# Kernel tuning notes

Measured on AMD Instinct MI355X. Metric: run time of the kernel, lower is better.

## Reference

```python
import jax, jax.numpy as jnp
import numpy as np

KS = 63      # Gaussian kernel size (module default)
SIGMA = 32.0 # Gaussian sigma (module default)


def _gaussian_kernel2d(k, sigma):
    # kornia get_gaussian_kernel2d: outer product of normalized 1D gaussians
    x = jnp.arange(k, dtype=jnp.float32) - k // 2
    g = jnp.exp(-(x * x) / (2.0 * sigma * sigma))
    g = g / g.sum()
    return jnp.outer(g, g)  # [k,k]


def _filter2d_constant(x, k2d):
    # kornia filter2d, border_type='constant' (zero pad), depthwise per channel
    C = x.shape[1]
    kern = jnp.broadcast_to(k2d, (C, 1) + k2d.shape)  # [C,1,k,k]
    return jax.lax.conv_general_dilated(
        x, kern, window_strides=(1, 1), padding='SAME',
        dimension_numbers=('NCHW', 'OIHW', 'NCHW'), feature_group_count=C)


def _grid_sample_bilinear(img, grid, align_corners=False):
    # torch.nn.functional.grid_sample, mode='bilinear', padding_mode='zeros'
    B, C, H, W = img.shape
    gx, gy = grid[..., 0], grid[..., 1]
    if align_corners:
        x = (gx + 1.0) * (W - 1) * 0.5
        y = (gy + 1.0) * (H - 1) * 0.5
    else:
        x = ((gx + 1.0) * W - 1.0) * 0.5
        y = ((gy + 1.0) * H - 1.0) * 0.5
    x0 = jnp.floor(x); y0 = jnp.floor(y)
    x0i = x0.astype(jnp.int32); y0i = y0.astype(jnp.int32)
    x1i = x0i + 1; y1i = y0i + 1
    wx1 = x - x0; wx0 = 1.0 - wx1
    wy1 = y - y0; wy0 = 1.0 - wy1

    def gather(iy, ix):
        valid = ((ix >= 0) & (ix < W) & (iy >= 0) & (iy < H))
        iyc = jnp.clip(iy, 0, H - 1)
        ixc = jnp.clip(ix, 0, W - 1)
        # per-batch fancy gather: [B,C,H,W]
        v = jax.vmap(lambda im, yy, xx: im[:, yy, xx])(img, iyc, ixc)
        return v * valid[:, None].astype(img.dtype)

    out = (gather(y0i, x0i) * (wy0 * wx0)[:, None]
           + gather(y0i, x1i) * (wy0 * wx1)[:, None]
           + gather(y1i, x0i) * (wy1 * wx0)[:, None]
           + gather(y1i, x1i) * (wy1 * wx1)[:, None])
    return out


def setup_inputs() -> dict:
    key = jax.random.key(0)
    k1, k2 = jax.random.split(key)
    image = jax.random.normal(k1, (8, 3, 512, 512), dtype=jnp.float32)
    noise = jax.random.uniform(k2, (8, 2, 512, 512), dtype=jnp.float32)
    return {"image": image, "noise": noise}


def reference(image, noise):
    B, C, H, W = image.shape
    noise = noise * 2.0 - 1.0                      # rand*2-1 as in forward()
    k2d = _gaussian_kernel2d(KS, SIGMA)
    disp_xy = _filter2d_constant(noise, k2d)       # [B,2,H,W]
    disp = jnp.transpose(disp_xy, (0, 2, 3, 1))    # [B,H,W,2] (x,y)
    # kornia create_meshgrid(normalized_coordinates=True): linspace(-1,1)
    xs = jnp.linspace(-1.0, 1.0, W, dtype=image.dtype)
    ys = jnp.linspace(-1.0, 1.0, H, dtype=image.dtype)
    base = jnp.stack(jnp.meshgrid(xs, ys, indexing='xy'), axis=-1)  # [H,W,2]
    grid = jnp.clip(base[None] + disp, -1.0, 1.0)
    warped = _grid_sample_bilinear(image, grid, align_corners=False)
    return warped, disp
```

## Files before the change

kernel.cpp:

```cpp
#include <hip/hip_runtime.h>
#include <math.h>

#define KS 63
#define RAD 31
#define NB 8
#define NC 3
#define NH 512
#define NW 512
#define PADH 576

struct GaussW { float w[KS]; };

__global__ __launch_bounds__(256) void hblur_kernel(const float* __restrict__ noise,
                                                    float* __restrict__ tmp, GaussW gw) {
    const int bid = blockIdx.x;
    const int t = threadIdx.x;
    if (bid >= NB * NH) {
        const int pid = bid - NB * NH;
        const int img = pid >> 5;
        const int pr  = pid & 31;
        const int row = (pr < 16) ? (pr * 2) : (544 + (pr - 16) * 2);
        float4* dst = (float4*)(tmp + ((size_t)img * PADH + row) * NW);
        dst[t] = make_float4(0.f, 0.f, 0.f, 0.f);
        return;
    }
    const int b = bid >> 9;
    const int h = bid & (NH - 1);
    const int ch = t >> 7;
    const int tt = t & 127;

    __shared__ float rows[2][PADH];
    const float* src = noise + ((size_t)(b * 2 + ch) * NH + h) * NW;
    {
        const float4 nv = *(const float4*)(src + 4 * tt);
        float4 sv;
        sv.x = fmaf(nv.x, 2.f, -1.f); sv.y = fmaf(nv.y, 2.f, -1.f);
        sv.z = fmaf(nv.z, 2.f, -1.f); sv.w = fmaf(nv.w, 2.f, -1.f);
        *(float4*)&rows[ch][32 + 4 * tt] = sv;
        if (tt < 8) {
            *(float4*)&rows[ch][4 * tt]       = make_float4(0.f, 0.f, 0.f, 0.f);
            *(float4*)&rows[ch][544 + 4 * tt] = make_float4(0.f, 0.f, 0.f, 0.f);
        }
    }
    __syncthreads();

    float acc[4] = {0.f, 0.f, 0.f, 0.f};
#pragma unroll
    for (int c = 0; c < 17; ++c) {
        const float4 v = *(const float4*)&rows[ch][4 * tt + 4 * c];
        const float vv[4] = {v.x, v.y, v.z, v.w};
#pragma unroll
        for (int e = 0; e < 4; ++e) {
#pragma unroll
            for (int oo = 0; oo < 4; ++oo) {
                const int j = 4 * c + e - oo - 1;
                if (j >= 0 && j < KS) acc[oo] = fmaf(vv[e], gw.w[j], acc[oo]);
            }
        }
    }
    float4* dst = (float4*)(tmp + (((size_t)(b * 2 + ch) * PADH) + 32 + h) * NW + 4 * tt);
    *dst = make_float4(acc[0], acc[1], acc[2], acc[3]);
}

__global__ __launch_bounds__(256) void vwarp_kernel(const float* __restrict__ tmp,
                                                    const float* __restrict__ img,
                                                    float2* __restrict__ disp,
                                                    float* __restrict__ warped,
                                                    GaussW gw) {
    const int t = threadIdx.x;
    int bid = blockIdx.x;
    bid = (bid & 7) * 256 + (bid >> 3);
    const int wt = bid & 1;
    const int ht = (bid >> 1) & 127;
    const int b  = bid >> 8;
    const int w  = wt * 256 + t;
    const int h0 = ht * 4;

    const float* c0 = tmp + (((size_t)(b * 2 + 0) * PADH) + h0 + 1) * NW + w;
    const float* c1 = tmp + (((size_t)(b * 2 + 1) * PADH) + h0 + 1) * NW + w;

    float ax[4] = {0.f, 0.f, 0.f, 0.f};
    float ay[4] = {0.f, 0.f, 0.f, 0.f};
#pragma unroll
    for (int rr = 0; rr < 66; ++rr) {
        const float vx = c0[(size_t)rr * NW];
        const float vy = c1[(size_t)rr * NW];
#pragma unroll
        for (int o = 0; o < 4; ++o) {
            const int j = rr - o;
            if (j >= 0 && j < KS) {
                ax[o] = fmaf(vx, gw.w[j], ax[o]);
                ay[o] = fmaf(vy, gw.w[j], ay[o]);
            }
        }
    }

    const float gxb = fmaf((float)w, 2.0f / 511.0f, -1.0f);
    const float* i0 = img + (size_t)b * NC * NH * NW;
    const float* i1 = i0 + NH * NW;
    const float* i2 = i1 + NH * NW;
    float* wp = warped + (size_t)b * NC * NH * NW;

#pragma unroll
    for (int o = 0; o < 4; ++o) {
        const int h = h0 + o;
        disp[((size_t)b * NH + h) * NW + w] = make_float2(ax[o], ay[o]);

        float gx = gxb + ax[o];
        float gy = fmaf((float)h, 2.0f / 511.0f, -1.0f) + ay[o];
        gx = fminf(1.f, fmaxf(-1.f, gx));
        gy = fminf(1.f, fmaxf(-1.f, gy));

        const float x = ((gx + 1.0f) * (float)NW - 1.0f) * 0.5f;
        const float y = ((gy + 1.0f) * (float)NH - 1.0f) * 0.5f;
        const float xf = floorf(x), yf = floorf(y);
        const int x0 = (int)xf, y0 = (int)yf;
        const int x1 = x0 + 1,  y1 = y0 + 1;
        const float wx1 = x - xf, wx0 = 1.0f - wx1;
        const float wy1 = y - yf, wy0 = 1.0f - wy1;
        const float fx0 = ((unsigned)x0 < NW) ? 1.f : 0.f;
        const float fx1 = ((unsigned)x1 < NW) ? 1.f : 0.f;
        const float fy0 = ((unsigned)y0 < NH) ? 1.f : 0.f;
        const float fy1 = ((unsigned)y1 < NH) ? 1.f : 0.f;
        const int x0c = min(max(x0, 0), NW - 1), x1c = min(max(x1, 0), NW - 1);
        const int y0c = min(max(y0, 0), NH - 1), y1c = min(max(y1, 0), NH - 1);
        const float w00 = wy0 * wx0 * (fy0 * fx0), w01 = wy0 * wx1 * (fy0 * fx1);
        const float w10 = wy1 * wx0 * (fy1 * fx0), w11 = wy1 * wx1 * (fy1 * fx1);
        const int o00 = y0c * NW + x0c, o01 = y0c * NW + x1c;
        const int o10 = y1c * NW + x0c, o11 = y1c * NW + x1c;
        const size_t po = (size_t)h * NW + w;
        wp[po]               = ((i0[o00] * w00 + i0[o01] * w01) + i0[o10] * w10) + i0[o11] * w11;
        wp[NH * NW + po]     = ((i1[o00] * w00 + i1[o01] * w01) + i1[o10] * w10) + i1[o11] * w11;
        wp[2 * NH * NW + po] = ((i2[o00] * w00 + i2[o01] * w01) + i2[o10] * w10) + i2[o11] * w11;
    }
}

extern "C" void kernel_launch(void* const* d_in, const int* in_sizes, int n_in,
                              void* d_out, int out_size, void* d_ws, size_t ws_size,
                              hipStream_t stream) {
    const float* image = (const float*)d_in[0];
    const float* noise = (const float*)d_in[1];
    float* warped = (float*)d_out;
    float* dispo  = (float*)d_out + (size_t)NB * NC * NH * NW;
    float* scratch = (float*)d_ws;

    GaussW gw;
    float s = 0.f;
    for (int i = 0; i < KS; ++i) {
        const float xv = (float)(i - RAD);
        gw.w[i] = expf(-(xv * xv) / (2.0f * 32.0f * 32.0f));
        s += gw.w[i];
    }
    for (int i = 0; i < KS; ++i) gw.w[i] /= s;

    hblur_kernel<<<NB * NH + 512, 256, 0, stream>>>(noise, scratch, gw);
    vwarp_kernel<<<NB * (NH / 4) * 2, 256, 0, stream>>>(scratch, image,
                                                        (float2*)dispo, warped, gw);
}
```

Baseline: 136.3 us.

## Split vertical blur and warp into separate kernels with float4 vectorization

The fused vertical-blur-plus-warp kernel is split in two. A vblur kernel handles 4 columns per thread with float4 loads and writes disp with vector stores, and a warp kernel reads disp back and computes 4 pixels per thread with float4 output stores. This aims to widen memory accesses and cut per-thread load instructions in the blur. The cost is an extra kernel launch, a round trip of disp through global memory, and vblur using only 512 blocks, which may under-occupy the GPU.

Measured after the change: 150.8 us. 10.7% more time.

```diff
diff --git a/kernel.cpp b/kernel.cpp
--- a/kernel.cpp
+++ b/kernel.cpp
@@ -62,52 +62,80 @@
     *dst = make_float4(acc[0], acc[1], acc[2], acc[3]);
 }
 
-__global__ __launch_bounds__(256) void vwarp_kernel(const float* __restrict__ tmp,
-                                                    const float* __restrict__ img,
-                                                    float2* __restrict__ disp,
-                                                    float* __restrict__ warped,
-                                                    GaussW gw) {
+__global__ __launch_bounds__(256) void vblur_kernel(const float* __restrict__ tmp,
+                                                    float2* __restrict__ disp, GaussW gw) {
     const int t = threadIdx.x;
     int bid = blockIdx.x;
-    bid = (bid & 7) * 256 + (bid >> 3);
-    const int wt = bid & 1;
-    const int ht = (bid >> 1) & 127;
-    const int b  = bid >> 8;
-    const int w  = wt * 256 + t;
-    const int h0 = ht * 4;
+    bid = (bid & 7) * 64 + (bid >> 3);
+    const int b  = bid >> 6;
+    const int hb = bid & 63;
+    const int wq = t & 127;
+    const int rg = t >> 7;
+    const int h0 = hb * 8 + rg * 4;
+    const int w4 = wq * 4;
 
-    const float* c0 = tmp + (((size_t)(b * 2 + 0) * PADH) + h0 + 1) * NW + w;
-    const float* c1 = tmp + (((size_t)(b * 2 + 1) * PADH) + h0 + 1) * NW + w;
+    const float* c0 = tmp + (((size_t)(b * 2 + 0) * PADH) + h0 + 1) * NW + w4;
+    const float* c1 = tmp + (((size_t)(b * 2 + 1) * PADH) + h0 + 1) * NW + w4;
 
-    float ax[4] = {0.f, 0.f, 0.f, 0.f};
-    float ay[4] = {0.f, 0.f, 0.f, 0.f};
+    float4 ax[4], ay[4];
+#pragma unroll
+    for (int o = 0; o < 4; ++o) {
+        ax[o] = make_float4(0.f, 0.f, 0.f, 0.f);
+        ay[o] = make_float4(0.f, 0.f, 0.f, 0.f);
+    }
 #pragma unroll
     for (int rr = 0; rr < 66; ++rr) {
-        const float vx = c0[(size_t)rr * NW];
-        const float vy = c1[(size_t)rr * NW];
+        const float4 vx = *(const float4*)(c0 + (size_t)rr * NW);
+        const float4 vy = *(const float4*)(c1 + (size_t)rr * NW);
 #pragma unroll
         for (int o = 0; o < 4; ++o) {
             const int j = rr - o;
             if (j >= 0 && j < KS) {
-                ax[o] = fmaf(vx, gw.w[j], ax[o]);
-                ay[o] = fmaf(vy, gw.w[j], ay[o]);
+                const float wj = gw.w[j];
+                ax[o].x = fmaf(vx.x, wj, ax[o].x); ax[o].y = fmaf(vx.y, wj, ax[o].y);
+                ax[o].z = fmaf(vx.z, wj, ax[o].z); ax[o].w = fmaf(vx.w, wj, ax[o].w);
+                ay[o].x = fmaf(vy.x, wj, ay[o].x); ay[o].y = fmaf(vy.y, wj, ay[o].y);
+                ay[o].z = fmaf(vy.z, wj, ay[o].z); ay[o].w = fmaf(vy.w, wj, ay[o].w);
             }
         }
     }
+#pragma unroll
+    for (int o = 0; o < 4; ++o) {
+        float2* row = disp + ((size_t)b * NH + h0 + o) * NW + w4;
+        *(float4*)(row)     = make_float4(ax[o].x, ay[o].x, ax[o].y, ay[o].y);
+        *(float4*)(row + 2) = make_float4(ax[o].z, ay[o].z, ax[o].w, ay[o].w);
+    }
+}
 
-    const float gxb = fmaf((float)w, 2.0f / 511.0f, -1.0f);
+__global__ __launch_bounds__(256) void warp_kernel(const float* __restrict__ img,
+                                                   const float2* __restrict__ disp,
+                                                   float* __restrict__ warped) {
+    const int t = threadIdx.x;
+    int bid = blockIdx.x;
+    bid = (bid & 7) * 256 + (bid >> 3);
+    const int b   = bid >> 8;
+    const int blk = bid & 255;
+    const int pix = blk * 1024 + t * 4;
+    const int h  = pix >> 9;
+    const int w0 = pix & 511;
+
+    const float2* dp = disp + (size_t)b * NH * NW + pix;
+    const float4 dA = *(const float4*)(dp);
+    const float4 dB = *(const float4*)(dp + 2);
+    const float dx[4] = {dA.x, dA.z, dB.x, dB.z};
+    const float dy[4] = {dA.y, dA.w, dB.y, dB.w};
+
     const float* i0 = img + (size_t)b * NC * NH * NW;
     const float* i1 = i0 + NH * NW;
     const float* i2 = i1 + NH * NW;
-    float* wp = warped + (size_t)b * NC * NH * NW;
+    float* wp = warped + (size_t)b * NC * NH * NW + pix;
 
+    const float gy0 = fmaf((float)h, 2.0f / 511.0f, -1.0f);
+    float o0[4], o1[4], o2[4];
 #pragma unroll
-    for (int o = 0; o < 4; ++o) {
-        const int h = h0 + o;
-        disp[((size_t)b * NH + h) * NW + w] = make_float2(ax[o], ay[o]);
-
-        float gx = gxb + ax[o];
-        float gy = fmaf((float)h, 2.0f / 511.0f, -1.0f) + ay[o];
+    for (int k = 0; k < 4; ++k) {
+        float gx = fmaf((float)(w0 + k), 2.0f / 511.0f, -1.0f) + dx[k];
+        float gy = gy0 + dy[k];
         gx = fminf(1.f, fmaxf(-1.f, gx));
         gy = fminf(1.f, fmaxf(-1.f, gy));
 
@@ -128,11 +156,13 @@
         const float w10 = wy1 * wx0 * (fy1 * fx0), w11 = wy1 * wx1 * (fy1 * fx1);
         const int o00 = y0c * NW + x0c, o01 = y0c * NW + x1c;
         const int o10 = y1c * NW + x0c, o11 = y1c * NW + x1c;
-        const size_t po = (size_t)h * NW + w;
-        wp[po]               = ((i0[o00] * w00 + i0[o01] * w01) + i0[o10] * w10) + i0[o11] * w11;
-        wp[NH * NW + po]     = ((i1[o00] * w00 + i1[o01] * w01) + i1[o10] * w10) + i1[o11] * w11;
-        wp[2 * NH * NW + po] = ((i2[o00] * w00 + i2[o01] * w01) + i2[o10] * w10) + i2[o11] * w11;
+        o0[k] = ((i0[o00] * w00 + i0[o01] * w01) + i0[o10] * w10) + i0[o11] * w11;
+        o1[k] = ((i1[o00] * w00 + i1[o01] * w01) + i1[o10] * w10) + i1[o11] * w11;
+        o2[k] = ((i2[o00] * w00 + i2[o01] * w01) + i2[o10] * w10) + i2[o11] * w11;
     }
+    *(float4*)(wp)                  = make_float4(o0[0], o0[1], o0[2], o0[3]);
+    *(float4*)(wp + NH * NW)        = make_float4(o1[0], o1[1], o1[2], o1[3]);
+    *(float4*)(wp + 2 * NH * NW)    = make_float4(o2[0], o2[1], o2[2], o2[3]);
 }
 
 extern "C" void kernel_launch(void* const* d_in, const int* in_sizes, int n_in,
@@ -154,6 +184,6 @@
     for (int i = 0; i < KS; ++i) gw.w[i] /= s;
 
     hblur_kernel<<<NB * NH + 512, 256, 0, stream>>>(noise, scratch, gw);
-    vwarp_kernel<<<NB * (NH / 4) * 2, 256, 0, stream>>>(scratch, image,
-                                                        (float2*)dispo, warped, gw);
+    vblur_kernel<<<512, 256, 0, stream>>>(scratch, (float2*)dispo, gw);
+    warp_kernel<<<2048, 256, 0, stream>>>(image, (const float2*)dispo, warped);
 }
```

## Stage vertical blur input tile in LDS to share rows across output rows

Applied to the files above, without the earlier changes.

The vertical blur/warp kernel now loads a 16x64 output tile's 78-row halo of the horizontally blurred field into shared memory, then each thread computes 4 rows from LDS. Before, each thread read 66 rows directly from global memory for only 4 outputs, so overlapping rows were fetched repeatedly. This cuts redundant global/L2 traffic. In exchange it adds about 40KB of LDS per block, which may limit occupancy, plus a barrier and narrower 64-wide image gather footprints.

Result: no change. 138.5 us (+1.6%).

```diff
diff --git a/kernel.cpp b/kernel.cpp
--- a/kernel.cpp
+++ b/kernel.cpp
@@ -8,6 +8,9 @@
 #define NH 512
 #define NW 512
 #define PADH 576
+#define TILE_H 16
+#define TILE_W 64
+#define ROWS 78
 
 struct GaussW { float w[KS]; };
 
@@ -70,21 +73,36 @@
     const int t = threadIdx.x;
     int bid = blockIdx.x;
     bid = (bid & 7) * 256 + (bid >> 3);
-    const int wt = bid & 1;
-    const int ht = (bid >> 1) & 127;
-    const int b  = bid >> 8;
-    const int w  = wt * 256 + t;
-    const int h0 = ht * 4;
+    const int b   = bid >> 8;
+    const int rem = bid & 255;
+    const int ht  = rem >> 3;
+    const int wt  = rem & 7;
+    const int H0 = ht * TILE_H;
+    const int W0 = wt * TILE_W;
 
-    const float* c0 = tmp + (((size_t)(b * 2 + 0) * PADH) + h0 + 1) * NW + w;
-    const float* c1 = tmp + (((size_t)(b * 2 + 1) * PADH) + h0 + 1) * NW + w;
+    __shared__ float lds[2][ROWS][TILE_W];
+
+    const float* g0 = tmp + ((size_t)(b * 2) * PADH + H0 + 1) * NW + W0;
+    const size_t choff = (size_t)PADH * NW;
+    for (int idx = t; idx < 2 * ROWS * (TILE_W / 4); idx += 256) {
+        const int l16  = idx & 15;
+        const int rowc = idx >> 4;
+        const int c = (rowc >= ROWS) ? 1 : 0;
+        const int r = rowc - ROWS * c;
+        const float4 v = *(const float4*)(g0 + (size_t)c * choff + (size_t)r * NW + l16 * 4);
+        *(float4*)&lds[c][r][l16 * 4] = v;
+    }
+    __syncthreads();
+
+    const int w  = t & 63;
+    const int lh = (t >> 6) * 4;
 
     float ax[4] = {0.f, 0.f, 0.f, 0.f};
     float ay[4] = {0.f, 0.f, 0.f, 0.f};
 #pragma unroll
     for (int rr = 0; rr < 66; ++rr) {
-        const float vx = c0[(size_t)rr * NW];
-        const float vy = c1[(size_t)rr * NW];
+        const float vx = lds[0][lh + rr][w];
+        const float vy = lds[1][lh + rr][w];
 #pragma unroll
         for (int o = 0; o < 4; ++o) {
             const int j = rr - o;
@@ -95,7 +113,8 @@
         }
     }
 
-    const float gxb = fmaf((float)w, 2.0f / 511.0f, -1.0f);
+    const int wg = W0 + w;
+    const float gxb = fmaf((float)wg, 2.0f / 511.0f, -1.0f);
     const float* i0 = img + (size_t)b * NC * NH * NW;
     const float* i1 = i0 + NH * NW;
     const float* i2 = i1 + NH * NW;
@@ -103,8 +122,8 @@
 
 #pragma unroll
     for (int o = 0; o < 4; ++o) {
-        const int h = h0 + o;
-        disp[((size_t)b * NH + h) * NW + w] = make_float2(ax[o], ay[o]);
+        const int h = H0 + lh + o;
+        disp[((size_t)b * NH + h) * NW + wg] = make_float2(ax[o], ay[o]);
 
         float gx = gxb + ax[o];
         float gy = fmaf((float)h, 2.0f / 511.0f, -1.0f) + ay[o];
@@ -128,7 +147,7 @@
         const float w10 = wy1 * wx0 * (fy1 * fx0), w11 = wy1 * wx1 * (fy1 * fx1);
         const int o00 = y0c * NW + x0c, o01 = y0c * NW + x1c;
         const int o10 = y1c * NW + x0c, o11 = y1c * NW + x1c;
-        const size_t po = (size_t)h * NW + w;
+        const size_t po = (size_t)h * NW + wg;
         wp[po]               = ((i0[o00] * w00 + i0[o01] * w01) + i0[o10] * w10) + i0[o11] * w11;
         wp[NH * NW + po]     = ((i1[o00] * w00 + i1[o01] * w01) + i1[o10] * w10) + i1[o11] * w11;
         wp[2 * NH * NW + po] = ((i2[o00] * w00 + i2[o01] * w01) + i2[o10] * w10) + i2[o11] * w11;
@@ -154,6 +173,6 @@
     for (int i = 0; i < KS; ++i) gw.w[i] /= s;
 
     hblur_kernel<<<NB * NH + 512, 256, 0, stream>>>(noise, scratch, gw);
-    vwarp_kernel<<<NB * (NH / 4) * 2, 256, 0, stream>>>(scratch, image,
-                                                        (float2*)dispo, warped, gw);
+    vwarp_kernel<<<NB * (NH / TILE_H) * (NW / TILE_W), 256, 0, stream>>>(
+        scratch, image, (float2*)dispo, warped, gw);
 }
```
